# Kernel optimization log

Measured on AMD Instinct MI355X. Metric: run time of the kernel, lower is better.

## Reference

```python
import jax, jax.numpy as jnp
import numpy as np

N_NODES = 50000
N_EDGES = 800000
DIM = 512
N_CLASSES = 1000


def _xavier(key, shape):
    fan_in, fan_out = shape[0], shape[1]
    lim = float(np.sqrt(6.0 / (fan_in + fan_out)))
    return jax.random.uniform(key, shape, jnp.float32, -lim, lim)


def setup_inputs() -> dict:
    key = jax.random.key(0)
    ks = jax.random.split(key, 12)
    nodes = jax.random.normal(ks[0], (N_NODES, DIM), jnp.float32)
    edges = jax.random.randint(ks[1], (2, N_EDGES), 0, N_NODES, jnp.int64)
    labelmatrix = jax.random.normal(ks[2], (N_CLASSES, 128), jnp.float32)
    return {
        "nodes": nodes,
        "edges": edges,
        "labelmatrix": labelmatrix,
        "W1": _xavier(ks[3], (DIM, 256)), "b1": jnp.zeros((256,), jnp.float32),
        "W2": _xavier(ks[4], (256, 192)), "b2": jnp.zeros((192,), jnp.float32),
        "W3": _xavier(ks[5], (192, 128)), "b3": jnp.zeros((128,), jnp.float32),
        "fc1_w": _xavier(ks[6], (128, 128)), "fc1_b": jnp.zeros((128,), jnp.float32),
        "fc2_w": _xavier(ks[7], (128, 128)), "fc2_b": jnp.zeros((128,), jnp.float32),
    }


def _gcn_conv(x, W, b, src, dst, n):
    # PyG GCNConv: add self-loops, symmetric normalization, then aggregate.
    xw = x @ W                                        # [N, out]
    ones = jnp.ones(src.shape[0], x.dtype)
    deg = jax.ops.segment_sum(ones, dst, num_segments=n) + 1.0  # +1 self-loop
    dinv = jax.lax.rsqrt(deg)                         # deg^{-1/2}
    coef = dinv[src] * dinv[dst]                      # [E]
    agg = jax.ops.segment_sum(xw[src] * coef[:, None], dst, num_segments=n)
    agg = agg + xw * (dinv * dinv)[:, None]           # self-loop contribution
    return agg + b


def reference(nodes, edges, labelmatrix, W1, b1, W2, b2, W3, b3,
              fc1_w, fc1_b, fc2_w, fc2_b):
    src, dst = edges[0], edges[1]
    n = nodes.shape[0]
    # _GraphConv: three stacked GCNConv layers, no inter-layer activation
    x = _gcn_conv(nodes, W1, b1, src, dst, n)
    x = _gcn_conv(x, W2, b2, src, dst, n)
    x = _gcn_conv(x, W3, b3, src, dst, n)             # [N, 128]
    # _GraphLinear (eval mode: dropout is identity)
    h = jax.nn.relu(x @ fc1_w + fc1_b)
    h = h @ fc2_w + fc2_b                             # [N, 128]
    preds = h @ labelmatrix.T                         # dot-product similarity [N, C]
    return preds
```

## Files before the change

### kernel.cpp

```cpp
#include <hip/hip_runtime.h>

typedef unsigned short u16;
typedef __bf16 bf16x8 __attribute__((ext_vector_type(8)));
typedef float f32x4 __attribute__((ext_vector_type(4)));

__device__ __forceinline__ u16 f2bf(float f) {
    unsigned int u = __float_as_uint(f);
    unsigned int r = (u + 0x7FFFu + ((u >> 16) & 1u)) >> 16;
    return (u16)r;
}
__device__ __forceinline__ float bf_lo(unsigned int u) { return __uint_as_float(u << 16); }
__device__ __forceinline__ float bf_hi(unsigned int u) { return __uint_as_float(u & 0xFFFF0000u); }

#define GLOAD_LDS(gp, lp) \
    __builtin_amdgcn_global_load_lds( \
        (const __attribute__((address_space(1))) unsigned int*)(gp), \
        (__attribute__((address_space(3))) unsigned int*)(lp), 16, 0, 0)


__global__ void hist_k(const int* __restrict__ dst, int* __restrict__ deg, int nE) {
    int e = blockIdx.x * 256 + threadIdx.x;
    if (e < nE) atomicAdd(&deg[dst[e]], 1);
}

__global__ void scan_block_k(const int* __restrict__ deg, int* __restrict__ scanned,
                             int* __restrict__ bsums, int n) {
    __shared__ int s[1024];
    int i = blockIdx.x * 1024 + threadIdx.x;
    int v = (i < n) ? deg[i] : 0;
    s[threadIdx.x] = v;
    __syncthreads();
    for (int off = 1; off < 1024; off <<= 1) {
        int t = (threadIdx.x >= off) ? s[threadIdx.x - off] : 0;
        __syncthreads();
        s[threadIdx.x] += t;
        __syncthreads();
    }
    if (i < n) scanned[i] = s[threadIdx.x];
    if (threadIdx.x == 1023) bsums[blockIdx.x] = s[1023];
}

__global__ void scan_final_dinv_k(const int* __restrict__ scanned, const int* __restrict__ deg,
                                  const int* __restrict__ bsums, int* __restrict__ rowptr,
                                  int* __restrict__ wptr, float* __restrict__ dinv,
                                  int n, int nE) {
    int i = blockIdx.x * 256 + threadIdx.x;
    if (i < n) {
        int pre = 0;
        int nbi = i >> 10;
        for (int j = 0; j < nbi; ++j) pre += bsums[j];
        int rp = scanned[i] - deg[i] + pre;
        rowptr[i] = rp;
        wptr[i] = rp;
        dinv[i] = rsqrtf((float)deg[i] + 1.0f);
    }
    if (i == 0) rowptr[n] = nE;
}

__global__ void csr_fill_k(const int* __restrict__ src, const int* __restrict__ dst,
                           int* __restrict__ wptr, const float* __restrict__ dinv,
                           int* __restrict__ eidx, float* __restrict__ ecoef, int nE) {
    int e = blockIdx.x * 256 + threadIdx.x;
    if (e >= nE) return;
    int d = dst[e], s = src[e];
    int p = atomicAdd(&wptr[d], 1);
    eidx[p] = s;
    ecoef[p] = dinv[s] * dinv[d];
}


__global__ __launch_bounds__(256) void prep_all_k(
    const float* __restrict__ W1, const float* __restrict__ W2, const float* __restrict__ W3,
    const float* __restrict__ b1, const float* __restrict__ b2,
    const float* __restrict__ fc1_w, const float* __restrict__ fc2_w,
    const float* __restrict__ fc2_b, const float* __restrict__ labelm,
    u16* __restrict__ Wp, float* __restrict__ c1, float* __restrict__ c2,
    u16* __restrict__ Bfc1, u16* __restrict__ Wc, float* __restrict__ bc) {
    __shared__ float lds[16706];
    const int b = blockIdx.x, tid = threadIdx.x;
    if (b < 512) {
        float* row = lds;
        float* t1r = lds + 256;
        row[tid] = (tid < 256) ? W1[b * 256 + tid] : 0.f;
        __syncthreads();
        if (tid < 192) {
            float s = 0.f;
            for (int k = 0; k < 256; ++k) s = fmaf(row[k], W2[k * 192 + tid], s);
            t1r[tid] = s;
        }
        __syncthreads();
        if (tid < 128) {
            float s = 0.f;
            for (int m = 0; m < 192; ++m) s = fmaf(t1r[m], W3[m * 128 + tid], s);
            Wp[(size_t)tid * 512 + b] = f2bf(s);
        }
    } else if (b == 512) {
        float* t1b = lds;
        if (tid < 192) {
            float s = 0.f;
            for (int k = 0; k < 256; ++k) s = fmaf(b1[k], W2[k * 192 + tid], s);
            t1b[tid] = s;
        }
        __syncthreads();
        if (tid < 128) {
            float a = 0.f, bb = 0.f;
            for (int m = 0; m < 192; ++m) {
                a  = fmaf(t1b[m], W3[m * 128 + tid], a);
                bb = fmaf(b2[m],  W3[m * 128 + tid], bb);
            }
            c1[tid] = a; c2[tid] = bb;
        }
    } else if (b < 577) {
        int idx = (b - 513) * 256 + tid;
        if (idx < 128 * 128) {
            int nn = idx >> 7, k = idx & 127;
            Bfc1[idx] = f2bf(fc1_w[k * 128 + nn]);
        }
    } else {
        const int cb = b - 577;
        float* w  = lds;
        float* lm = lds + 16512;
        float* red = lds + 16640;
        for (int t = tid; t < 128 * 128; t += 256)
            w[(t >> 7) * 129 + (t & 127)] = fc2_w[t];
        __syncthreads();
        for (int cc = 0; cc < 8; ++cc) {
            int c = cb * 8 + cc;
            if (tid < 128) lm[tid] = (c < 1000) ? labelm[(size_t)c * 128 + tid] : 0.f;
            __syncthreads();
            if (tid < 128) {
                float sum = 0.f;
                const float* wr = &w[tid * 129];
                for (int j = 0; j < 128; ++j) sum = fmaf(wr[j], lm[j], sum);
                Wc[(size_t)c * 128 + tid] = f2bf(sum);
                float p = fc2_b[tid] * lm[tid];
                for (int off = 32; off > 0; off >>= 1) p += __shfl_down(p, off);
                if ((tid & 63) == 0) red[tid >> 6] = p;
            }
            __syncthreads();
            if (tid == 0) bc[c] = red[0] + red[1];
            __syncthreads();
        }
    }
}


template <bool CASTA, bool OUTF32, bool BIAS, bool RELU>
__global__ __launch_bounds__(256) void gemm_mfma(
    const void* __restrict__ Ap, const u16* __restrict__ Bt,
    const float* __restrict__ bias, void* __restrict__ Cout,
    int K, int Nout, int ldc, int Mout, int lgny, int Arows) {
    __shared__ __align__(16) u16 As[128 * 64];
    __shared__ __align__(16) u16 Bs[128 * 64];
    const int tid  = threadIdx.x;
    const int lane = tid & 63;
    const int w    = tid >> 6;
    const int wm   = w >> 1, wn = w & 1;

    const int nwg = gridDim.x, orig = blockIdx.x;
    const int q = nwg >> 3, r = nwg & 7;
    const int xcd = orig & 7, off = orig >> 3;
    const int tile = (xcd < r ? xcd * (q + 1) : r * (q + 1) + (xcd - r) * q) + off;
    const int ny = 1 << lgny;
    const int tx = tile >> lgny, ty = tile & (ny - 1);
    const size_t bm = (size_t)tx * 128;
    const size_t bn = (size_t)ty * 128;

    const int l7 = lane & 7;
    const int l3 = lane >> 3;
    const int kcs = l7 ^ l3;

    f32x4 acc[4][4] = {};

    for (int k0 = 0; k0 < K; k0 += 64) {
        if constexpr (CASTA) {
            const float* Af = (const float*)Ap;
            const int row = tid >> 1;
            const int half = tid & 1;
            const size_t grow = bm + row;
            const bool valid = grow < (size_t)Arows;
            const float4* g4 = (const float4*)(Af + grow * K + k0 + half * 32);
            float4 f[8];
#pragma unroll
            for (int j = 0; j < 8; ++j)
                f[j] = valid ? g4[j] : make_float4(0.f, 0.f, 0.f, 0.f);
#pragma unroll
            for (int j = 0; j < 4; ++j) {
                int kc = (half * 4 + j) ^ (row & 7);
                uint4 o;
                o.x = (unsigned)f2bf(f[2 * j].x)     | ((unsigned)f2bf(f[2 * j].y) << 16);
                o.y = (unsigned)f2bf(f[2 * j].z)     | ((unsigned)f2bf(f[2 * j].w) << 16);
                o.z = (unsigned)f2bf(f[2 * j + 1].x) | ((unsigned)f2bf(f[2 * j + 1].y) << 16);
                o.w = (unsigned)f2bf(f[2 * j + 1].z) | ((unsigned)f2bf(f[2 * j + 1].w) << 16);
                *(uint4*)((char*)As + row * 128 + kc * 16) = o;
            }
#pragma unroll
            for (int it = 0; it < 4; ++it) {
                const int r0 = w * 32 + it * 8;
                const u16* gB = Bt + ((size_t)(bn + r0 + l3) * K + k0) + kcs * 8;
                GLOAD_LDS(gB, Bs + r0 * 64);
            }
        } else {
            const u16* A = (const u16*)Ap;
#pragma unroll
            for (int it = 0; it < 4; ++it) {
                const int r0 = w * 32 + it * 8;
                const u16* gA = A + ((size_t)(bm + r0 + l3) * K + k0) + kcs * 8;
                GLOAD_LDS(gA, As + r0 * 64);
                const u16* gB = Bt + ((size_t)(bn + r0 + l3) * K + k0) + kcs * 8;
                GLOAD_LDS(gB, Bs + r0 * 64);
            }
        }
        __syncthreads();

#pragma unroll
        for (int ks = 0; ks < 2; ++ks) {
            bf16x8 av[4], bv[4];
#pragma unroll
            for (int i = 0; i < 4; ++i) {
                int row = wm * 64 + i * 16 + (lane & 15);
                int kc = (ks * 4 + (lane >> 4)) ^ (lane & 7);
                av[i] = *(const bf16x8*)((const char*)As + row * 128 + kc * 16);
            }
#pragma unroll
            for (int j = 0; j < 4; ++j) {
                int nn = wn * 64 + j * 16 + (lane & 15);
                int kc = (ks * 4 + (lane >> 4)) ^ (lane & 7);
                bv[j] = *(const bf16x8*)((const char*)Bs + nn * 128 + kc * 16);
            }
#pragma unroll
            for (int i = 0; i < 4; ++i)
#pragma unroll
                for (int j = 0; j < 4; ++j)
                    acc[i][j] = __builtin_amdgcn_mfma_f32_16x16x32_bf16(av[i], bv[j], acc[i][j], 0, 0, 0);
        }
        __syncthreads();
    }

    const int ccol  = lane & 15;
    const int crow4 = (lane >> 4) * 4;
#pragma unroll
    for (int i = 0; i < 4; ++i) {
#pragma unroll
        for (int j = 0; j < 4; ++j) {
#pragma unroll
            for (int r2 = 0; r2 < 4; ++r2) {
                size_t gr = bm + wm * 64 + i * 16 + crow4 + r2;
                size_t gc = bn + wn * 64 + j * 16 + ccol;
                if (gr < (size_t)Mout && gc < (size_t)Nout) {
                    float v = acc[i][j][r2];
                    if constexpr (BIAS) v += bias[gc];
                    if constexpr (RELU) v = fmaxf(v, 0.f);
                    if constexpr (OUTF32) ((float*)Cout)[gr * ldc + gc] = v;
                    else                  ((u16*)Cout)[gr * ldc + gc] = f2bf(v);
                }
            }
        }
    }
}


template <int MODE>
__global__ __launch_bounds__(256) void agg128_k(
    const u16* __restrict__ xw, const int* __restrict__ rowptr,
    const int* __restrict__ eidx, const float* __restrict__ ecoef,
    const float* __restrict__ dinv, u16* __restrict__ out,
    float* __restrict__ u1, const float* __restrict__ c1,
    const float* __restrict__ c2, const float* __restrict__ b3, int n) {
    const int tid = threadIdx.x;
    const int sub = tid >> 4;
    const int fl  = tid & 15;
    int node = blockIdx.x * 16 + sub;
    if (node >= n) return;

    const uint4* xv = (const uint4*)xw;
    float di = dinv[node];
    float s = di * di;
    uint4 a = xv[(size_t)node * 16 + fl];
    float acc[8];
    acc[0] = s * bf_lo(a.x); acc[1] = s * bf_hi(a.x);
    acc[2] = s * bf_lo(a.y); acc[3] = s * bf_hi(a.y);
    acc[4] = s * bf_lo(a.z); acc[5] = s * bf_hi(a.z);
    acc[6] = s * bf_lo(a.w); acc[7] = s * bf_hi(a.w);
    float usum = 0.f;

    const int beg = rowptr[node], end = rowptr[node + 1];
    int e = beg;
    for (; e + 7 < end; e += 8) {
        int sn[8]; float cf[8]; uint4 v[8];
#pragma unroll
        for (int q = 0; q < 8; ++q) { sn[q] = eidx[e + q]; cf[q] = ecoef[e + q]; }
#pragma unroll
        for (int q = 0; q < 8; ++q) v[q] = xv[(size_t)sn[q] * 16 + fl];
#pragma unroll
        for (int q = 0; q < 8; ++q) {
            if constexpr (MODE == 0) usum += cf[q];
            if constexpr (MODE == 2) usum = fmaf(cf[q], u1[sn[q]], usum);
            acc[0] = fmaf(cf[q], bf_lo(v[q].x), acc[0]); acc[1] = fmaf(cf[q], bf_hi(v[q].x), acc[1]);
            acc[2] = fmaf(cf[q], bf_lo(v[q].y), acc[2]); acc[3] = fmaf(cf[q], bf_hi(v[q].y), acc[3]);
            acc[4] = fmaf(cf[q], bf_lo(v[q].z), acc[4]); acc[5] = fmaf(cf[q], bf_hi(v[q].z), acc[5]);
            acc[6] = fmaf(cf[q], bf_lo(v[q].w), acc[6]); acc[7] = fmaf(cf[q], bf_hi(v[q].w), acc[7]);
        }
    }
    for (; e < end; ++e) {
        int sn = eidx[e];
        float c = ecoef[e];
        uint4 v = xv[(size_t)sn * 16 + fl];
        if constexpr (MODE == 0) usum += c;
        if constexpr (MODE == 2) usum = fmaf(c, u1[sn], usum);
        acc[0] = fmaf(c, bf_lo(v.x), acc[0]); acc[1] = fmaf(c, bf_hi(v.x), acc[1]);
        acc[2] = fmaf(c, bf_lo(v.y), acc[2]); acc[3] = fmaf(c, bf_hi(v.y), acc[3]);
        acc[4] = fmaf(c, bf_lo(v.z), acc[4]); acc[5] = fmaf(c, bf_hi(v.z), acc[5]);
        acc[6] = fmaf(c, bf_lo(v.w), acc[6]); acc[7] = fmaf(c, bf_hi(v.w), acc[7]);
    }

    if constexpr (MODE == 0) {
        if (fl == 0) u1[node] = s + usum;
    }
    if constexpr (MODE == 2) {
        float u1n = u1[node];
        float u2n = s * u1n + usum;
        float4 c1a = ((const float4*)c1)[fl * 2], c1b = ((const float4*)c1)[fl * 2 + 1];
        float4 c2a = ((const float4*)c2)[fl * 2], c2b = ((const float4*)c2)[fl * 2 + 1];
        float4 b3a = ((const float4*)b3)[fl * 2], b3b = ((const float4*)b3)[fl * 2 + 1];
        acc[0] += u2n * c1a.x + u1n * c2a.x + b3a.x;
        acc[1] += u2n * c1a.y + u1n * c2a.y + b3a.y;
        acc[2] += u2n * c1a.z + u1n * c2a.z + b3a.z;
        acc[3] += u2n * c1a.w + u1n * c2a.w + b3a.w;
        acc[4] += u2n * c1b.x + u1n * c2b.x + b3b.x;
        acc[5] += u2n * c1b.y + u1n * c2b.y + b3b.y;
        acc[6] += u2n * c1b.z + u1n * c2b.z + b3b.z;
        acc[7] += u2n * c1b.w + u1n * c2b.w + b3b.w;
    }

    uint4 o;
    o.x = (unsigned)f2bf(acc[0]) | ((unsigned)f2bf(acc[1]) << 16);
    o.y = (unsigned)f2bf(acc[2]) | ((unsigned)f2bf(acc[3]) << 16);
    o.z = (unsigned)f2bf(acc[4]) | ((unsigned)f2bf(acc[5]) << 16);
    o.w = (unsigned)f2bf(acc[6]) | ((unsigned)f2bf(acc[7]) << 16);
    ((uint4*)out)[(size_t)node * 16 + fl] = o;
}


extern "C" void kernel_launch(void* const* d_in, const int* in_sizes, int n_in,
                              void* d_out, int out_size, void* d_ws, size_t ws_size,
                              hipStream_t stream) {
    const float* nodes  = (const float*)d_in[0];
    const int*   edges  = (const int*)d_in[1];
    const float* labelm = (const float*)d_in[2];
    const float* W1 = (const float*)d_in[3];
    const float* b1 = (const float*)d_in[4];
    const float* W2 = (const float*)d_in[5];
    const float* b2 = (const float*)d_in[6];
    const float* W3 = (const float*)d_in[7];
    const float* b3 = (const float*)d_in[8];
    const float* fc1_w = (const float*)d_in[9];
    const float* fc1_b = (const float*)d_in[10];
    const float* fc2_w = (const float*)d_in[11];
    const float* fc2_b = (const float*)d_in[12];
    float* out = (float*)d_out;

    const int DIM = 512, N3 = 128, NC = 1000;
    const int n  = in_sizes[0] / DIM;
    const int nE = in_sizes[1] / 2;
    const int Mpad = 50048;
    const int* src = edges;
    const int* dst = edges + nE;

    u16* Y = (u16*)((char*)d_out + 67108864);
    u16* Z = (u16*)((char*)d_out + 100663296);

    char* ws = (char*)d_ws;
    u16*   Q      = (u16*)(ws);
    u16*   Rb     = (u16*)(ws + 12812288);
    u16*   Wp     = (u16*)(ws + 26017792);
    u16*   Bfc1   = (u16*)(ws + 26148864);
    u16*   Wc     = (u16*)(ws + 26181632);
    float* bc     = (float*)(ws + 26443776);
    float* c1     = (float*)(ws + 26447872);
    float* c2     = (float*)(ws + 26448384);
    float* u1     = (float*)(ws + 26448896);
    int*   deg_i  = (int*)(ws + 26848896);
    float* dinv   = (float*)(ws + 27048896);
    int*   rowptr = (int*)(ws + 27248896);
    int*   wptr   = (int*)(ws + 27448960);
    int*   scanned= (int*)(ws + 27648960);
    int*   bsums  = (int*)(ws + 27848960);
    int*   eidx   = (int*)(ws + 27849216);
    float* ecoef  = (float*)(ws + 31049216);

    hipMemsetAsync(deg_i, 0, (size_t)n * 4, stream);
    hist_k<<<(nE + 255) / 256, 256, 0, stream>>>(dst, deg_i, nE);
    int nb = (n + 1023) / 1024;
    scan_block_k<<<nb, 1024, 0, stream>>>(deg_i, scanned, bsums, n);
    scan_final_dinv_k<<<(n + 255) / 256, 256, 0, stream>>>(scanned, deg_i, bsums, rowptr, wptr, dinv, n, nE);
    csr_fill_k<<<(nE + 255) / 256, 256, 0, stream>>>(src, dst, wptr, dinv, eidx, ecoef, nE);

    prep_all_k<<<705, 256, 0, stream>>>(W1, W2, W3, b1, b2, fc1_w, fc2_w, fc2_b, labelm,
                                        Wp, c1, c2, Bfc1, Wc, bc);

    const int gx = Mpad / 128;
    dim3 blk(256);
    const int gagg = (n + 15) / 16;

    gemm_mfma<true, false, false, false><<<gx, blk, 0, stream>>>(nodes, Wp, nullptr, Y, 512, N3, N3, Mpad, 0, n);
    agg128_k<0><<<gagg, blk, 0, stream>>>(Y, rowptr, eidx, ecoef, dinv, Z, u1, nullptr, nullptr, nullptr, n);
    agg128_k<1><<<gagg, blk, 0, stream>>>(Z, rowptr, eidx, ecoef, dinv, Y, nullptr, nullptr, nullptr, nullptr, n);
    agg128_k<2><<<gagg, blk, 0, stream>>>(Y, rowptr, eidx, ecoef, dinv, Rb, u1, c1, c2, b3, n);
    gemm_mfma<false, false, true, true><<<gx, blk, 0, stream>>>(Rb, Bfc1, fc1_b, Q, 128, N3, N3, Mpad, 0, Mpad);
    gemm_mfma<false, true, true, false><<<gx * 8, blk, 0, stream>>>(Q, Wc, bc, out, 128, NC, NC, n, 3, Mpad);
}
```

Measured before the change: 371.0 us.

## Co-schedule independent preprocessing kernels in shared launches to cut launch count

Independent kernels are merged by splitting the block range of a single launch. The degree histogram shares a launch with the weight-folding prep, the scan with the fc2/label folding, and the CSR fill with the first GEMM. This cuts launch overhead and lets independent work run concurrently on idle CUs. The cost is larger static LDS for the scan blocks and non-uniform block roles inside each launch.

```diff
diff --git a/kernel.cpp b/kernel.cpp
--- a/kernel.cpp
+++ b/kernel.cpp
@@ -18,27 +18,112 @@
         (__attribute__((address_space(3))) unsigned int*)(lp), 16, 0, 0)
 
 
-__global__ void hist_k(const int* __restrict__ dst, int* __restrict__ deg, int nE) {
-    int e = blockIdx.x * 256 + threadIdx.x;
-    if (e < nE) atomicAdd(&deg[dst[e]], 1);
-}
-
-__global__ void scan_block_k(const int* __restrict__ deg, int* __restrict__ scanned,
-                             int* __restrict__ bsums, int n) {
-    __shared__ int s[1024];
-    int i = blockIdx.x * 1024 + threadIdx.x;
-    int v = (i < n) ? deg[i] : 0;
-    s[threadIdx.x] = v;
+__global__ __launch_bounds__(256) void hist_prep_k(
+    const int* __restrict__ dst, int* __restrict__ deg, int nE,
+    const float* __restrict__ W1, const float* __restrict__ W2, const float* __restrict__ W3,
+    const float* __restrict__ b1, const float* __restrict__ b2,
+    const float* __restrict__ fc1_w,
+    u16* __restrict__ Wp, float* __restrict__ c1, float* __restrict__ c2,
+    u16* __restrict__ Bfc1, int nbHist) {
+    __shared__ float lds[448];
+    const int b = blockIdx.x, tid = threadIdx.x;
+    if (b < nbHist) {
+        int e = b * 256 + tid;
+        if (e < nE) atomicAdd(&deg[dst[e]], 1);
+        return;
+    }
+    const int b2i = b - nbHist;
+    if (b2i < 512) {
+        float* row = lds;
+        float* t1r = lds + 256;
+        row[tid & 255] = (tid < 256) ? W1[b2i * 256 + tid] : 0.f;
+        __syncthreads();
+        if (tid < 192) {
+            float s = 0.f;
+            for (int k = 0; k < 256; ++k) s = fmaf(row[k], W2[k * 192 + tid], s);
+            t1r[tid] = s;
+        }
+        __syncthreads();
+        if (tid < 128) {
+            float s = 0.f;
+            for (int m = 0; m < 192; ++m) s = fmaf(t1r[m], W3[m * 128 + tid], s);
+            Wp[(size_t)tid * 512 + b2i] = f2bf(s);
+        }
+    } else if (b2i == 512) {
+        float* t1b = lds;
+        if (tid < 192) {
+            float s = 0.f;
+            for (int k = 0; k < 256; ++k) s = fmaf(b1[k], W2[k * 192 + tid], s);
+            t1b[tid] = s;
+        }
+        __syncthreads();
+        if (tid < 128) {
+            float a = 0.f, bb = 0.f;
+            for (int m = 0; m < 192; ++m) {
+                a  = fmaf(t1b[m], W3[m * 128 + tid], a);
+                bb = fmaf(b2[m],  W3[m * 128 + tid], bb);
+            }
+            c1[tid] = a; c2[tid] = bb;
+        }
+    } else {
+        int idx = (b2i - 513) * 256 + tid;
+        if (idx < 128 * 128) {
+            int nn = idx >> 7, k = idx & 127;
+            Bfc1[idx] = f2bf(fc1_w[k * 128 + nn]);
+        }
+    }
+}
+
+
+__global__ __launch_bounds__(1024) void scan_fc2_k(
+    const int* __restrict__ deg, int* __restrict__ scanned, int* __restrict__ bsums, int n,
+    const float* __restrict__ fc2_w, const float* __restrict__ fc2_b,
+    const float* __restrict__ labelm, u16* __restrict__ Wc, float* __restrict__ bc,
+    int nbScan) {
+    __shared__ char smem[66824];
+    const int b = blockIdx.x, tid = threadIdx.x;
+    if (b < nbScan) {
+        int* s = (int*)smem;
+        int i = b * 1024 + tid;
+        int v = (i < n) ? deg[i] : 0;
+        s[tid] = v;
+        __syncthreads();
+        for (int off = 1; off < 1024; off <<= 1) {
+            int t = (tid >= off) ? s[tid - off] : 0;
+            __syncthreads();
+            s[tid] += t;
+            __syncthreads();
+        }
+        if (i < n) scanned[i] = s[tid];
+        if (tid == 1023) bsums[b] = s[1023];
+        return;
+    }
+    const int cb = b - nbScan;
+    float* w   = (float*)smem;
+    float* lm  = (float*)smem + 16512;
+    float* red = (float*)smem + 16640;
+    for (int t = tid; t < 128 * 128; t += 1024)
+        w[(t >> 7) * 129 + (t & 127)] = fc2_w[t];
     __syncthreads();
-    for (int off = 1; off < 1024; off <<= 1) {
-        int t = (threadIdx.x >= off) ? s[threadIdx.x - off] : 0;
-        __syncthreads();
-        s[threadIdx.x] += t;
-        __syncthreads();
-    }
-    if (i < n) scanned[i] = s[threadIdx.x];
-    if (threadIdx.x == 1023) bsums[blockIdx.x] = s[1023];
-}
+    for (int cc = 0; cc < 8; ++cc) {
+        int c = cb * 8 + cc;
+        if (tid < 128) lm[tid] = (c < 1000) ? labelm[(size_t)c * 128 + tid] : 0.f;
+        __syncthreads();
+        if (tid < 128) {
+            float sum = 0.f;
+            const float* wr = &w[tid * 129];
+            for (int j = 0; j < 128; ++j) sum = fmaf(wr[j], lm[j], sum);
+            Wc[(size_t)c * 128 + tid] = f2bf(sum);
+            float p = fc2_b[tid] * lm[tid];
+            for (int off = 32; off > 0; off >>= 1) p += __shfl_down(p, off);
+            if ((tid & 63) == 0) red[tid >> 6] = p;
+        }
+        __syncthreads();
+        if (tid == 0) bc[c] = red[0] + red[1];
+        __syncthreads();
+    }
+}
+
 
 __global__ void scan_final_dinv_k(const int* __restrict__ scanned, const int* __restrict__ deg,
                                   const int* __restrict__ bsums, int* __restrict__ rowptr,
@@ -57,99 +142,105 @@
     if (i == 0) rowptr[n] = nE;
 }
 
-__global__ void csr_fill_k(const int* __restrict__ src, const int* __restrict__ dst,
-                           int* __restrict__ wptr, const float* __restrict__ dinv,
-                           int* __restrict__ eidx, float* __restrict__ ecoef, int nE) {
-    int e = blockIdx.x * 256 + threadIdx.x;
-    if (e >= nE) return;
-    int d = dst[e], s = src[e];
-    int p = atomicAdd(&wptr[d], 1);
-    eidx[p] = s;
-    ecoef[p] = dinv[s] * dinv[d];
-}
-
-
-__global__ __launch_bounds__(256) void prep_all_k(
-    const float* __restrict__ W1, const float* __restrict__ W2, const float* __restrict__ W3,
-    const float* __restrict__ b1, const float* __restrict__ b2,
-    const float* __restrict__ fc1_w, const float* __restrict__ fc2_w,
-    const float* __restrict__ fc2_b, const float* __restrict__ labelm,
-    u16* __restrict__ Wp, float* __restrict__ c1, float* __restrict__ c2,
-    u16* __restrict__ Bfc1, u16* __restrict__ Wc, float* __restrict__ bc) {
-    __shared__ float lds[16706];
+
+__global__ __launch_bounds__(256) void fill_gemmY_k(
+    const int* __restrict__ src, const int* __restrict__ dst,
+    int* __restrict__ wptr, const float* __restrict__ dinv,
+    int* __restrict__ eidx, float* __restrict__ ecoef, int nE,
+    const float* __restrict__ Af, const u16* __restrict__ Bt,
+    u16* __restrict__ Y, int Arows, int nbFill) {
+    __shared__ __align__(16) u16 As[128 * 64];
+    __shared__ __align__(16) u16 Bs[128 * 64];
     const int b = blockIdx.x, tid = threadIdx.x;
-    if (b < 512) {
-        float* row = lds;
-        float* t1r = lds + 256;
-        row[tid] = (tid < 256) ? W1[b * 256 + tid] : 0.f;
-        __syncthreads();
-        if (tid < 192) {
-            float s = 0.f;
-            for (int k = 0; k < 256; ++k) s = fmaf(row[k], W2[k * 192 + tid], s);
-            t1r[tid] = s;
-        }
-        __syncthreads();
-        if (tid < 128) {
-            float s = 0.f;
-            for (int m = 0; m < 192; ++m) s = fmaf(t1r[m], W3[m * 128 + tid], s);
-            Wp[(size_t)tid * 512 + b] = f2bf(s);
-        }
-    } else if (b == 512) {
-        float* t1b = lds;
-        if (tid < 192) {
-            float s = 0.f;
-            for (int k = 0; k < 256; ++k) s = fmaf(b1[k], W2[k * 192 + tid], s);
-            t1b[tid] = s;
-        }
-        __syncthreads();
-        if (tid < 128) {
-            float a = 0.f, bb = 0.f;
-            for (int m = 0; m < 192; ++m) {
-                a  = fmaf(t1b[m], W3[m * 128 + tid], a);
-                bb = fmaf(b2[m],  W3[m * 128 + tid], bb);
-            }
-            c1[tid] = a; c2[tid] = bb;
-        }
-    } else if (b < 577) {
-        int idx = (b - 513) * 256 + tid;
-        if (idx < 128 * 128) {
-            int nn = idx >> 7, k = idx & 127;
-            Bfc1[idx] = f2bf(fc1_w[k * 128 + nn]);
-        }
-    } else {
-        const int cb = b - 577;
-        float* w  = lds;
-        float* lm = lds + 16512;
-        float* red = lds + 16640;
-        for (int t = tid; t < 128 * 128; t += 256)
-            w[(t >> 7) * 129 + (t & 127)] = fc2_w[t];
-        __syncthreads();
-        for (int cc = 0; cc < 8; ++cc) {
-            int c = cb * 8 + cc;
-            if (tid < 128) lm[tid] = (c < 1000) ? labelm[(size_t)c * 128 + tid] : 0.f;
-            __syncthreads();
-            if (tid < 128) {
-                float sum = 0.f;
-                const float* wr = &w[tid * 129];
-                for (int j = 0; j < 128; ++j) sum = fmaf(wr[j], lm[j], sum);
-                Wc[(size_t)c * 128 + tid] = f2bf(sum);
-                float p = fc2_b[tid] * lm[tid];
-                for (int off = 32; off > 0; off >>= 1) p += __shfl_down(p, off);
-                if ((tid & 63) == 0) red[tid >> 6] = p;
-            }
-            __syncthreads();
-            if (tid == 0) bc[c] = red[0] + red[1];
-            __syncthreads();
-        }
-    }
-}
-
-
-template <bool CASTA, bool OUTF32, bool BIAS, bool RELU>
+    if (b < nbFill) {
+        int e = b * 256 + tid;
+        if (e < nE) {
+            int d = dst[e], s = src[e];
+            int p = atomicAdd(&wptr[d], 1);
+            eidx[p] = s;
+            ecoef[p] = dinv[s] * dinv[d];
+        }
+        return;
+    }
+    const int lane = tid & 63;
+    const int w    = tid >> 6;
+    const int wm   = w >> 1, wn = w & 1;
+    const size_t bm = (size_t)(b - nbFill) * 128;
+    const int l7 = lane & 7, l3 = lane >> 3;
+    const int kcs = l7 ^ l3;
+    const int K = 512;
+
+    f32x4 acc[4][4] = {};
+    for (int k0 = 0; k0 < K; k0 += 64) {
+        const int row = tid >> 1;
+        const int half = tid & 1;
+        const size_t grow = bm + row;
+        const bool valid = grow < (size_t)Arows;
+        const float4* g4 = (const float4*)(Af + grow * K + k0 + half * 32);
+        float4 f[8];
+#pragma unroll
+        for (int j = 0; j < 8; ++j)
+            f[j] = valid ? g4[j] : make_float4(0.f, 0.f, 0.f, 0.f);
+#pragma unroll
+        for (int j = 0; j < 4; ++j) {
+            int kc = (half * 4 + j) ^ (row & 7);
+            uint4 o;
+            o.x = (unsigned)f2bf(f[2 * j].x)     | ((unsigned)f2bf(f[2 * j].y) << 16);
+            o.y = (unsigned)f2bf(f[2 * j].z)     | ((unsigned)f2bf(f[2 * j].w) << 16);
+            o.z = (unsigned)f2bf(f[2 * j + 1].x) | ((unsigned)f2bf(f[2 * j + 1].y) << 16);
+            o.w = (unsigned)f2bf(f[2 * j + 1].z) | ((unsigned)f2bf(f[2 * j + 1].w) << 16);
+            *(uint4*)((char*)As + row * 128 + kc * 16) = o;
+        }
+#pragma unroll
+        for (int it = 0; it < 4; ++it) {
+            const int r0 = w * 32 + it * 8;
+            const u16* gB = Bt + ((size_t)(r0 + l3) * K + k0) + kcs * 8;
+            GLOAD_LDS(gB, Bs + r0 * 64);
+        }
+        __syncthreads();
+#pragma unroll
+        for (int ks = 0; ks < 2; ++ks) {
+            bf16x8 av[4], bv[4];
+#pragma unroll
+            for (int i = 0; i < 4; ++i) {
+                int rr = wm * 64 + i * 16 + (lane & 15);
+                int kc = (ks * 4 + (lane >> 4)) ^ (lane & 7);
+                av[i] = *(const bf16x8*)((const char*)As + rr * 128 + kc * 16);
+            }
+#pragma unroll
+            for (int j = 0; j < 4; ++j) {
+                int nn = wn * 64 + j * 16 + (lane & 15);
+                int kc = (ks * 4 + (lane >> 4)) ^ (lane & 7);
+                bv[j] = *(const bf16x8*)((const char*)Bs + nn * 128 + kc * 16);
+            }
+#pragma unroll
+            for (int i = 0; i < 4; ++i)
+#pragma unroll
+                for (int j = 0; j < 4; ++j)
+                    acc[i][j] = __builtin_amdgcn_mfma_f32_16x16x32_bf16(av[i], bv[j], acc[i][j], 0, 0, 0);
+        }
+        __syncthreads();
+    }
+    const int ccol  = lane & 15;
+    const int crow4 = (lane >> 4) * 4;
+#pragma unroll
+    for (int i = 0; i < 4; ++i)
+#pragma unroll
+        for (int j = 0; j < 4; ++j)
+#pragma unroll
+            for (int r2 = 0; r2 < 4; ++r2) {
+                size_t gr = bm + wm * 64 + i * 16 + crow4 + r2;
+                size_t gc = wn * 64 + j * 16 + ccol;
+                Y[gr * 128 + gc] = f2bf(acc[i][j][r2]);
+            }
+}
+
+
+template <bool OUTF32, bool BIAS, bool RELU>
 __global__ __launch_bounds__(256) void gemm_mfma(
-    const void* __restrict__ Ap, const u16* __restrict__ Bt,
+    const u16* __restrict__ A, const u16* __restrict__ Bt,
     const float* __restrict__ bias, void* __restrict__ Cout,
-    int K, int Nout, int ldc, int Mout, int lgny, int Arows) {
+    int K, int Nout, int ldc, int Mout, int lgny) {
     __shared__ __align__(16) u16 As[128 * 64];
     __shared__ __align__(16) u16 Bs[128 * 64];
     const int tid  = threadIdx.x;
@@ -173,43 +264,13 @@
     f32x4 acc[4][4] = {};
 
     for (int k0 = 0; k0 < K; k0 += 64) {
-        if constexpr (CASTA) {
-            const float* Af = (const float*)Ap;
-            const int row = tid >> 1;
-            const int half = tid & 1;
-            const size_t grow = bm + row;
-            const bool valid = grow < (size_t)Arows;
-            const float4* g4 = (const float4*)(Af + grow * K + k0 + half * 32);
-            float4 f[8];
-#pragma unroll
-            for (int j = 0; j < 8; ++j)
-                f[j] = valid ? g4[j] : make_float4(0.f, 0.f, 0.f, 0.f);
-#pragma unroll
-            for (int j = 0; j < 4; ++j) {
-                int kc = (half * 4 + j) ^ (row & 7);
-                uint4 o;
-                o.x = (unsigned)f2bf(f[2 * j].x)     | ((unsigned)f2bf(f[2 * j].y) << 16);
-                o.y = (unsigned)f2bf(f[2 * j].z)     | ((unsigned)f2bf(f[2 * j].w) << 16);
-                o.z = (unsigned)f2bf(f[2 * j + 1].x) | ((unsigned)f2bf(f[2 * j + 1].y) << 16);
-                o.w = (unsigned)f2bf(f[2 * j + 1].z) | ((unsigned)f2bf(f[2 * j + 1].w) << 16);
-                *(uint4*)((char*)As + row * 128 + kc * 16) = o;
-            }
-#pragma unroll
-            for (int it = 0; it < 4; ++it) {
-                const int r0 = w * 32 + it * 8;
-                const u16* gB = Bt + ((size_t)(bn + r0 + l3) * K + k0) + kcs * 8;
-                GLOAD_LDS(gB, Bs + r0 * 64);
-            }
-        } else {
-            const u16* A = (const u16*)Ap;
-#pragma unroll
-            for (int it = 0; it < 4; ++it) {
-                const int r0 = w * 32 + it * 8;
-                const u16* gA = A + ((size_t)(bm + r0 + l3) * K + k0) + kcs * 8;
-                GLOAD_LDS(gA, As + r0 * 64);
-                const u16* gB = Bt + ((size_t)(bn + r0 + l3) * K + k0) + kcs * 8;
-                GLOAD_LDS(gB, Bs + r0 * 64);
-            }
+#pragma unroll
+        for (int it = 0; it < 4; ++it) {
+            const int r0 = w * 32 + it * 8;
+            const u16* gA = A + ((size_t)(bm + r0 + l3) * K + k0) + kcs * 8;
+            GLOAD_LDS(gA, As + r0 * 64);
+            const u16* gB = Bt + ((size_t)(bn + r0 + l3) * K + k0) + kcs * 8;
+            GLOAD_LDS(gB, Bs + r0 * 64);
         }
         __syncthreads();
 
@@ -389,24 +450,23 @@
     int*   eidx   = (int*)(ws + 27849216);
     float* ecoef  = (float*)(ws + 31049216);
 
+    const int nbHist = (nE + 255) / 256;
+    const int nbScan = (n + 1023) / 1024;
+    const int gx = Mpad / 128;
+    const int gagg = (n + 15) / 16;
+    dim3 blk(256);
+
     hipMemsetAsync(deg_i, 0, (size_t)n * 4, stream);
-    hist_k<<<(nE + 255) / 256, 256, 0, stream>>>(dst, deg_i, nE);
-    int nb = (n + 1023) / 1024;
-    scan_block_k<<<nb, 1024, 0, stream>>>(deg_i, scanned, bsums, n);
-    scan_final_dinv_k<<<(n + 255) / 256, 256, 0, stream>>>(scanned, deg_i, bsums, rowptr, wptr, dinv, n, nE);
-    csr_fill_k<<<(nE + 255) / 256, 256, 0, stream>>>(src, dst, wptr, dinv, eidx, ecoef, nE);
-
-    prep_all_k<<<705, 256, 0, stream>>>(W1, W2, W3, b1, b2, fc1_w, fc2_w, fc2_b, labelm,
-                                        Wp, c1, c2, Bfc1, Wc, bc);
-
-    const int gx = Mpad / 128;
-    dim3 blk(256);
-    const int gagg = (n + 15) / 16;
-
-    gemm_mfma<true, false, false, false><<<gx, blk, 0, stream>>>(nodes, Wp, nullptr, Y, 512, N3, N3, Mpad, 0, n);
+    hist_prep_k<<<nbHist + 577, blk, 0, stream>>>(dst, deg_i, nE, W1, W2, W3, b1, b2,
+                                                  fc1_w, Wp, c1, c2, Bfc1, nbHist);
+    scan_fc2_k<<<nbScan + 128, 1024, 0, stream>>>(deg_i, scanned, bsums, n,
+                                                  fc2_w, fc2_b, labelm, Wc, bc, nbScan);
+    scan_final_dinv_k<<<(n + 255) / 256, blk, 0, stream>>>(scanned, deg_i, bsums, rowptr, wptr, dinv, n, nE);
+    fill_gemmY_k<<<nbHist + gx, blk, 0, stream>>>(src, dst, wptr, dinv, eidx, ecoef, nE,
+                                                  nodes, Wp, Y, n, nbHist);
     agg128_k<0><<<gagg, blk, 0, stream>>>(Y, rowptr, eidx, ecoef, dinv, Z, u1, nullptr, nullptr, nullptr, n);
     agg128_k<1><<<gagg, blk, 0, stream>>>(Z, rowptr, eidx, ecoef, dinv, Y, nullptr, nullptr, nullptr, nullptr, n);
     agg128_k<2><<<gagg, blk, 0, stream>>>(Y, rowptr, eidx, ecoef, dinv, Rb, u1, c1, c2, b3, n);
-    gemm_mfma<false, false, true, true><<<gx, blk, 0, stream>>>(Rb, Bfc1, fc1_b, Q, 128, N3, N3, Mpad, 0, Mpad);
-    gemm_mfma<false, true, true, false><<<gx * 8, blk, 0, stream>>>(Q, Wc, bc, out, 128, NC, NC, n, 3, Mpad);
-}
+    gemm_mfma<false, true, true><<<gx, blk, 0, stream>>>(Rb, Bfc1, fc1_b, Q, 128, N3, N3, Mpad, 0);
+    gemm_mfma<true, true, false><<<gx * 8, blk, 0, stream>>>(Q, Wc, bc, out, 128, NC, NC, n, 3);
+}
```

Result: no change. 376.8 us (+1.6%).
